# Performance work log

Hardware: AMD Instinct MI355X
Metric: run time of the kernel (lower is better)

Reference implementation:

```python
import jax, jax.numpy as jnp
import numpy as np

NUM_MEMORIES = 4096
HIDDEN_DIM = 64
TEMPERATURE = 0.5
SHRINK_THRES = 0.0025
EPS = 1e-12


def _l2_normalize(v, axis=-1):
    # matches torch F.normalize: v / max(||v||_2, eps)
    n = jnp.sqrt(jnp.sum(v * v, axis=axis, keepdims=True))
    return v / jnp.maximum(n, EPS)


def _hard_shrink_relu(w, lambd):
    # relu(w - lambd) * w / (|w - lambd| + eps)
    d = w - lambd
    return jax.nn.relu(d) * w / (jnp.abs(d) + EPS)


def setup_inputs() -> dict:
    key = jax.random.key(0)
    kx, km = jax.random.split(key)
    x = jax.random.normal(kx, (16, 2048, HIDDEN_DIM), dtype=jnp.float32)
    # xavier_uniform for (num_memories, hidden_dim)
    bound = float(np.sqrt(6.0 / (NUM_MEMORIES + HIDDEN_DIM)))
    memories = jax.random.uniform(km, (NUM_MEMORIES, HIDDEN_DIM), dtype=jnp.float32,
                                  minval=-bound, maxval=bound)
    return {"x": x, "memories": memories}


def reference(x, memories):
    # cosine similarity addressing
    x_n = _l2_normalize(x, axis=-1)                      # [B,S,D]
    m_n = _l2_normalize(memories, axis=-1)               # [M,D]
    logits = jnp.einsum('bsd,md->bsm', x_n, m_n)         # [B,S,M]
    weight = jax.nn.softmax(logits / TEMPERATURE, axis=-1)
    # hard-shrink sparsification + L1 renormalization
    weight = _hard_shrink_relu(weight, SHRINK_THRES)
    l1 = jnp.sum(jnp.abs(weight), axis=-1, keepdims=True)
    weight = weight / jnp.maximum(l1, EPS)
    read = jnp.einsum('bsm,md->bsd', weight, memories)   # [B,S,D]
    return read, weight
```

## Files before the change

### kernel.cpp

```cpp
#include <hip/hip_runtime.h>
#include <hip/hip_bf16.h>


#define NM 4096
#define HD 64
#define NROWS 32768

typedef short bf16x8 __attribute__((ext_vector_type(8)));
typedef float f32x4  __attribute__((ext_vector_type(4)));

__global__ __launch_bounds__(256) void prep_rows(const float* __restrict__ src,
                                                 ushort* __restrict__ dst,
                                                 float scale) {
    const int wave = threadIdx.x >> 6, lane = threadIdx.x & 63;
    const long row = (long)blockIdx.x * 4 + wave;
    float v = src[row * HD + lane];
    float s = v * v;
#pragma unroll
    for (int o = 32; o; o >>= 1) s += __shfl_xor(s, o, 64);
    const float inv = scale / fmaxf(sqrtf(s), 1e-12f);
    __hip_bfloat16 h = __float2bfloat16(v * inv);
    dst[row * HD + lane] = *reinterpret_cast<ushort*>(&h);
}

__global__ __launch_bounds__(256) void prep_m_swz(const float* __restrict__ mem,
                                                  ushort* __restrict__ mbs) {
    const int wave = threadIdx.x >> 6, lane = threadIdx.x & 63;
    const int row = blockIdx.x * 4 + wave;
    float v = mem[row * HD + lane];
    float s = v * v;
#pragma unroll
    for (int o = 32; o; o >>= 1) s += __shfl_xor(s, o, 64);
    const float inv = 1.0f / fmaxf(sqrtf(s), 1e-12f);
    __hip_bfloat16 h = __float2bfloat16(v * inv);
    const int t = row >> 4, c = row & 15;
    const int k = lane;
    const int f = k >> 5, q = (k >> 3) & 3, j = k & 7;
    mbs[(long)t * 1024 + f * 512 + (q * 16 + c) * 8 + j] =
        *reinterpret_cast<ushort*>(&h);
}

__global__ __launch_bounds__(256, 2) void fused_gate(const ushort* __restrict__ xb,
                                                     const ushort* __restrict__ mbs,
                                                     const float* __restrict__ mem,
                                                     float* __restrict__ out_w,
                                                     float* __restrict__ out_read) {
    const int wv = threadIdx.x >> 6, lane = threadIdx.x & 63;
    const int q = lane >> 4, c = lane & 15;
    const int m0 = blockIdx.x * 16;
    const int nbase = wv * 1024;

    __shared__ float sS[4][16];
    __shared__ float sL[4][16];
    __shared__ float sred[4][16][64];
    __shared__ float tile[4][16][68];

    const bf16x8 a0 = *(const bf16x8*)(xb + (long)(m0 + c) * HD + q * 8);
    const bf16x8 a1 = *(const bf16x8*)(xb + (long)(m0 + c) * HD + q * 8 + 32);
    const ushort* mstrip = mbs + (long)(wv * 64) * 1024;

    float tmax[64];
    float sm[4] = {0.0f, 0.0f, 0.0f, 0.0f};
#pragma unroll 4
    for (int i = 0; i < 64; i++) {
        const ushort* mc = mstrip + (long)i * 1024 + lane * 8;
        const bf16x8 b0 = *(const bf16x8*)(mc);
        const bf16x8 b1 = *(const bf16x8*)(mc + 512);
        f32x4 t = {0.0f, 0.0f, 0.0f, 0.0f};
        t = __builtin_amdgcn_mfma_f32_16x16x32_bf16(a0, b0, t, 0, 0, 0);
        t = __builtin_amdgcn_mfma_f32_16x16x32_bf16(a1, b1, t, 0, 0, 0);
        tmax[i] = fmaxf(fmaxf(t[0], t[1]), fmaxf(t[2], t[3]));
#pragma unroll
        for (int r = 0; r < 4; r++) sm[r] += __expf(t[r]);
    }
#pragma unroll
    for (int o = 1; o < 16; o <<= 1)
#pragma unroll
        for (int r = 0; r < 4; r++) sm[r] += __shfl_xor(sm[r], o, 64);
    if (c == 0)
#pragma unroll
        for (int r = 0; r < 4; r++) sS[wv][q * 4 + r] = sm[r];
    __syncthreads();
    float rS[4], tmin = 1e30f;
#pragma unroll
    for (int r = 0; r < 4; r++) {
        const float S = sS[0][q * 4 + r] + sS[1][q * 4 + r] +
                        sS[2][q * 4 + r] + sS[3][q * 4 + r];
        rS[r] = 1.0f / S;
        const float tau = __logf(0.0025f * S) - 1e-3f;
        tmin = fminf(tmin, tau);
    }

    float l1[4] = {0.0f, 0.0f, 0.0f, 0.0f};
    for (int i = 0; i < 64; i++) {
        if (__ballot(tmax[i] > tmin)) {
            const ushort* mc = mstrip + (long)i * 1024 + lane * 8;
            const bf16x8 b0 = *(const bf16x8*)(mc);
            const bf16x8 b1 = *(const bf16x8*)(mc + 512);
            f32x4 t = {0.0f, 0.0f, 0.0f, 0.0f};
            t = __builtin_amdgcn_mfma_f32_16x16x32_bf16(a0, b0, t, 0, 0, 0);
            t = __builtin_amdgcn_mfma_f32_16x16x32_bf16(a1, b1, t, 0, 0, 0);
#pragma unroll
            for (int r = 0; r < 4; r++) {
                float w  = __expf(t[r]) * rS[r];
                float d  = w - 0.0025f;
                l1[r] += __fdividef(fmaxf(d, 0.0f) * w, fabsf(d) + 1e-12f);
            }
        }
    }
#pragma unroll
    for (int o = 1; o < 16; o <<= 1)
#pragma unroll
        for (int r = 0; r < 4; r++) l1[r] += __shfl_xor(l1[r], o, 64);
    if (c == 0)
#pragma unroll
        for (int r = 0; r < 4; r++) sL[wv][q * 4 + r] = l1[r];
    __syncthreads();
    float rL[4];
#pragma unroll
    for (int r = 0; r < 4; r++)
        rL[r] = 1.0f / fmaxf(sL[0][q * 4 + r] + sL[1][q * 4 + r] +
                             sL[2][q * 4 + r] + sL[3][q * 4 + r], 1e-12f);

    float racc[16];
#pragma unroll
    for (int r = 0; r < 16; r++) racc[r] = 0.0f;
    const int row_t = lane >> 4;
    const int c4    = lane & 15;
    const float4 z4 = make_float4(0.0f, 0.0f, 0.0f, 0.0f);

    for (int g = 0; g < 16; g++) {
        unsigned long long dirty = 0;
#pragma unroll
        for (int ii = 0; ii < 4; ii++)
            dirty |= __ballot(tmax[g * 4 + ii] > tmin);
        const int gbase = nbase + g * 64;

        if (!dirty) {
#pragma unroll
            for (int s = 0; s < 4; s++) {
                const int row = s * 4 + row_t;
                *(float4*)(out_w + (long)(m0 + row) * NM + gbase + c4 * 4) = z4;
            }
            continue;
        }

#pragma unroll
        for (int ii = 0; ii < 4; ii++) {
            const int i  = g * 4 + ii;
            const int n0 = nbase + i * 16;
            const ushort* mc = mstrip + (long)i * 1024 + lane * 8;
            const bf16x8 b0 = *(const bf16x8*)(mc);
            const bf16x8 b1 = *(const bf16x8*)(mc + 512);
            f32x4 t = {0.0f, 0.0f, 0.0f, 0.0f};
            t = __builtin_amdgcn_mfma_f32_16x16x32_bf16(a0, b0, t, 0, 0, 0);
            t = __builtin_amdgcn_mfma_f32_16x16x32_bf16(a1, b1, t, 0, 0, 0);
            float wf[4];
#pragma unroll
            for (int r = 0; r < 4; r++) {
                float w  = __expf(t[r]) * rS[r];
                float d  = w - 0.0025f;
                float sh = __fdividef(fmaxf(d, 0.0f) * w, fabsf(d) + 1e-12f);
                wf[r] = sh * rL[r];
                tile[wv][q * 4 + r][ii * 16 + c] = wf[r];
            }

            const bool nz = (wf[0] != 0.0f) | (wf[1] != 0.0f) |
                            (wf[2] != 0.0f) | (wf[3] != 0.0f);
            unsigned long long mask = __ballot(nz);
            while (mask) {
                const int j = __ffsll((long long)mask) - 1;
                mask &= (mask - 1);
                const int qj = j >> 4, cj = j & 15;
                float b0v = __shfl(wf[0], j, 64), b1v = __shfl(wf[1], j, 64);
                float b2v = __shfl(wf[2], j, 64), b3v = __shfl(wf[3], j, 64);
                const float mv = mem[(long)(n0 + cj) * HD + lane];
                switch (qj) {
                    case 0: racc[0]  += b0v * mv; racc[1]  += b1v * mv;
                            racc[2]  += b2v * mv; racc[3]  += b3v * mv; break;
                    case 1: racc[4]  += b0v * mv; racc[5]  += b1v * mv;
                            racc[6]  += b2v * mv; racc[7]  += b3v * mv; break;
                    case 2: racc[8]  += b0v * mv; racc[9]  += b1v * mv;
                            racc[10] += b2v * mv; racc[11] += b3v * mv; break;
                    default: racc[12] += b0v * mv; racc[13] += b1v * mv;
                             racc[14] += b2v * mv; racc[15] += b3v * mv; break;
                }
            }
        }

        __asm__ volatile("s_waitcnt lgkmcnt(0)" ::: "memory");
#pragma unroll
        for (int s = 0; s < 4; s++) {
            const int row = s * 4 + row_t;
            float4 v = *(const float4*)&tile[wv][row][c4 * 4];
            *(float4*)(out_w + (long)(m0 + row) * NM + gbase + c4 * 4) = v;
        }
    }

#pragma unroll
    for (int r = 0; r < 16; r++) sred[wv][r][lane] = racc[r];
    __syncthreads();
#pragma unroll
    for (int rr = 0; rr < 4; rr++) {
        const int row = wv * 4 + rr;
        const float v = sred[0][row][lane] + sred[1][row][lane] +
                        sred[2][row][lane] + sred[3][row][lane];
        out_read[(long)(m0 + row) * HD + lane] = v;
    }
}

extern "C" void kernel_launch(void* const* d_in, const int* in_sizes, int n_in,
                              void* d_out, int out_size, void* d_ws, size_t ws_size,
                              hipStream_t stream) {
    const float* x   = (const float*)d_in[0];
    const float* mem = (const float*)d_in[1];
    ushort* xb       = (ushort*)d_ws;
    ushort* mbs      = xb + (long)NROWS * HD;
    float* out_read  = (float*)d_out;
    float* out_w     = out_read + (long)NROWS * HD;

    prep_rows<<<NROWS / 4, 256, 0, stream>>>(x, xb, 2.0f);
    prep_m_swz<<<NM / 4, 256, 0, stream>>>(mem, mbs);
    fused_gate<<<NROWS / 16, 256, 0, stream>>>(xb, mbs, mem, out_w, out_read);
}
```

Measured before the change: 618.8 us.

## Split fused gate kernel into stats pass and separate weight-write pass

The fused kernel is split into two kernels. k_stats computes the softmax sums, L1 norms and the read output, keeps only one tile max per pair of tiles to save registers, and raises the occupancy hint to 3. It also saves per-row stats and per-wave group masks to workspace. k_write then recomputes the logits for dirty groups and streams the dense weight matrix, with a coalesced fast path for all-zero blocks. The aim is to overlap the large output store with less register pressure, at the cost of an extra launch and recomputing the matmul for dirty groups.

```diff
diff --git a/kernel.cpp b/kernel.cpp
--- a/kernel.cpp
+++ b/kernel.cpp
@@ -40,11 +40,12 @@
         *reinterpret_cast<ushort*>(&h);
 }
 
-__global__ __launch_bounds__(256, 2) void fused_gate(const ushort* __restrict__ xb,
-                                                     const ushort* __restrict__ mbs,
-                                                     const float* __restrict__ mem,
-                                                     float* __restrict__ out_w,
-                                                     float* __restrict__ out_read) {
+__global__ __launch_bounds__(256, 3) void k_stats(const ushort* __restrict__ xb,
+                                                  const ushort* __restrict__ mbs,
+                                                  const float* __restrict__ mem,
+                                                  float2* __restrict__ stats,
+                                                  uint* __restrict__ masks,
+                                                  float* __restrict__ out_read) {
     const int wv = threadIdx.x >> 6, lane = threadIdx.x & 63;
     const int q = lane >> 4, c = lane & 15;
     const int m0 = blockIdx.x * 16;
@@ -53,25 +54,39 @@
     __shared__ float sS[4][16];
     __shared__ float sL[4][16];
     __shared__ float sred[4][16][64];
-    __shared__ float tile[4][16][68];
 
     const bf16x8 a0 = *(const bf16x8*)(xb + (long)(m0 + c) * HD + q * 8);
     const bf16x8 a1 = *(const bf16x8*)(xb + (long)(m0 + c) * HD + q * 8 + 32);
     const ushort* mstrip = mbs + (long)(wv * 64) * 1024;
 
-    float tmax[64];
+    float tmax2[32];
     float sm[4] = {0.0f, 0.0f, 0.0f, 0.0f};
-#pragma unroll 4
-    for (int i = 0; i < 64; i++) {
-        const ushort* mc = mstrip + (long)i * 1024 + lane * 8;
-        const bf16x8 b0 = *(const bf16x8*)(mc);
-        const bf16x8 b1 = *(const bf16x8*)(mc + 512);
-        f32x4 t = {0.0f, 0.0f, 0.0f, 0.0f};
-        t = __builtin_amdgcn_mfma_f32_16x16x32_bf16(a0, b0, t, 0, 0, 0);
-        t = __builtin_amdgcn_mfma_f32_16x16x32_bf16(a1, b1, t, 0, 0, 0);
-        tmax[i] = fmaxf(fmaxf(t[0], t[1]), fmaxf(t[2], t[3]));
-#pragma unroll
-        for (int r = 0; r < 4; r++) sm[r] += __expf(t[r]);
+#pragma unroll 2
+    for (int p = 0; p < 32; p++) {
+        float tm;
+        {
+            const ushort* mc = mstrip + (long)(2 * p) * 1024 + lane * 8;
+            const bf16x8 b0 = *(const bf16x8*)(mc);
+            const bf16x8 b1 = *(const bf16x8*)(mc + 512);
+            f32x4 t = {0.0f, 0.0f, 0.0f, 0.0f};
+            t = __builtin_amdgcn_mfma_f32_16x16x32_bf16(a0, b0, t, 0, 0, 0);
+            t = __builtin_amdgcn_mfma_f32_16x16x32_bf16(a1, b1, t, 0, 0, 0);
+            tm = fmaxf(fmaxf(t[0], t[1]), fmaxf(t[2], t[3]));
+#pragma unroll
+            for (int r = 0; r < 4; r++) sm[r] += __expf(t[r]);
+        }
+        {
+            const ushort* mc = mstrip + (long)(2 * p + 1) * 1024 + lane * 8;
+            const bf16x8 b0 = *(const bf16x8*)(mc);
+            const bf16x8 b1 = *(const bf16x8*)(mc + 512);
+            f32x4 t = {0.0f, 0.0f, 0.0f, 0.0f};
+            t = __builtin_amdgcn_mfma_f32_16x16x32_bf16(a0, b0, t, 0, 0, 0);
+            t = __builtin_amdgcn_mfma_f32_16x16x32_bf16(a1, b1, t, 0, 0, 0);
+            tm = fmaxf(tm, fmaxf(fmaxf(t[0], t[1]), fmaxf(t[2], t[3])));
+#pragma unroll
+            for (int r = 0; r < 4; r++) sm[r] += __expf(t[r]);
+        }
+        tmax2[p] = tm;
     }
 #pragma unroll
     for (int o = 1; o < 16; o <<= 1)
@@ -92,19 +107,22 @@
     }
 
     float l1[4] = {0.0f, 0.0f, 0.0f, 0.0f};
-    for (int i = 0; i < 64; i++) {
-        if (__ballot(tmax[i] > tmin)) {
-            const ushort* mc = mstrip + (long)i * 1024 + lane * 8;
-            const bf16x8 b0 = *(const bf16x8*)(mc);
-            const bf16x8 b1 = *(const bf16x8*)(mc + 512);
-            f32x4 t = {0.0f, 0.0f, 0.0f, 0.0f};
-            t = __builtin_amdgcn_mfma_f32_16x16x32_bf16(a0, b0, t, 0, 0, 0);
-            t = __builtin_amdgcn_mfma_f32_16x16x32_bf16(a1, b1, t, 0, 0, 0);
-#pragma unroll
-            for (int r = 0; r < 4; r++) {
-                float w  = __expf(t[r]) * rS[r];
-                float d  = w - 0.0025f;
-                l1[r] += __fdividef(fmaxf(d, 0.0f) * w, fabsf(d) + 1e-12f);
+    for (int p = 0; p < 32; p++) {
+        if (__ballot(tmax2[p] > tmin)) {
+#pragma unroll
+            for (int h = 0; h < 2; h++) {
+                const ushort* mc = mstrip + (long)(2 * p + h) * 1024 + lane * 8;
+                const bf16x8 b0 = *(const bf16x8*)(mc);
+                const bf16x8 b1 = *(const bf16x8*)(mc + 512);
+                f32x4 t = {0.0f, 0.0f, 0.0f, 0.0f};
+                t = __builtin_amdgcn_mfma_f32_16x16x32_bf16(a0, b0, t, 0, 0, 0);
+                t = __builtin_amdgcn_mfma_f32_16x16x32_bf16(a1, b1, t, 0, 0, 0);
+#pragma unroll
+                for (int r = 0; r < 4; r++) {
+                    float w = __expf(t[r]) * rS[r];
+                    float d = w - 0.0025f;
+                    l1[r] += __fdividef(fmaxf(d, 0.0f) * w, fabsf(d) + 1e-12f);
+                }
             }
         }
     }
@@ -121,30 +139,20 @@
     for (int r = 0; r < 4; r++)
         rL[r] = 1.0f / fmaxf(sL[0][q * 4 + r] + sL[1][q * 4 + r] +
                              sL[2][q * 4 + r] + sL[3][q * 4 + r], 1e-12f);
+    if (wv == 0 && c == 0)
+#pragma unroll
+        for (int r = 0; r < 4; r++)
+            stats[m0 + q * 4 + r] = make_float2(rS[r], rL[r]);
 
     float racc[16];
 #pragma unroll
     for (int r = 0; r < 16; r++) racc[r] = 0.0f;
-    const int row_t = lane >> 4;
-    const int c4    = lane & 15;
-    const float4 z4 = make_float4(0.0f, 0.0f, 0.0f, 0.0f);
-
+    uint gm = 0;
     for (int g = 0; g < 16; g++) {
-        unsigned long long dirty = 0;
-#pragma unroll
-        for (int ii = 0; ii < 4; ii++)
-            dirty |= __ballot(tmax[g * 4 + ii] > tmin);
-        const int gbase = nbase + g * 64;
-
-        if (!dirty) {
-#pragma unroll
-            for (int s = 0; s < 4; s++) {
-                const int row = s * 4 + row_t;
-                *(float4*)(out_w + (long)(m0 + row) * NM + gbase + c4 * 4) = z4;
-            }
-            continue;
-        }
-
+        unsigned long long d0 = __ballot(tmax2[2 * g] > tmin);
+        unsigned long long d1 = __ballot(tmax2[2 * g + 1] > tmin);
+        if (!(d0 | d1)) continue;
+        gm |= 1u << g;
 #pragma unroll
         for (int ii = 0; ii < 4; ii++) {
             const int i  = g * 4 + ii;
@@ -162,9 +170,7 @@
                 float d  = w - 0.0025f;
                 float sh = __fdividef(fmaxf(d, 0.0f) * w, fabsf(d) + 1e-12f);
                 wf[r] = sh * rL[r];
-                tile[wv][q * 4 + r][ii * 16 + c] = wf[r];
-            }
-
+            }
             const bool nz = (wf[0] != 0.0f) | (wf[1] != 0.0f) |
                             (wf[2] != 0.0f) | (wf[3] != 0.0f);
             unsigned long long mask = __ballot(nz);
@@ -187,15 +193,8 @@
                 }
             }
         }
-
-        __asm__ volatile("s_waitcnt lgkmcnt(0)" ::: "memory");
-#pragma unroll
-        for (int s = 0; s < 4; s++) {
-            const int row = s * 4 + row_t;
-            float4 v = *(const float4*)&tile[wv][row][c4 * 4];
-            *(float4*)(out_w + (long)(m0 + row) * NM + gbase + c4 * 4) = v;
-        }
-    }
+    }
+    if (lane == 0) masks[blockIdx.x * 4 + wv] = gm;
 
 #pragma unroll
     for (int r = 0; r < 16; r++) sred[wv][r][lane] = racc[r];
@@ -206,6 +205,81 @@
         const float v = sred[0][row][lane] + sred[1][row][lane] +
                         sred[2][row][lane] + sred[3][row][lane];
         out_read[(long)(m0 + row) * HD + lane] = v;
+    }
+}
+
+__global__ __launch_bounds__(256) void k_write(const ushort* __restrict__ xb,
+                                               const ushort* __restrict__ mbs,
+                                               const float2* __restrict__ stats,
+                                               const uint* __restrict__ masks,
+                                               float* __restrict__ out_w) {
+    const int tid = threadIdx.x;
+    const int wv = tid >> 6, lane = tid & 63;
+    const int q = lane >> 4, c = lane & 15;
+    const int m0 = blockIdx.x * 16;
+
+    __shared__ uint sgm[4];
+    __shared__ float tile[4][16][68];
+
+    if (tid < 4) sgm[tid] = masks[blockIdx.x * 4 + tid];
+    __syncthreads();
+    const uint any = sgm[0] | sgm[1] | sgm[2] | sgm[3];
+    const float4 z4 = make_float4(0.0f, 0.0f, 0.0f, 0.0f);
+
+    if (!any) {
+        float4* base = (float4*)(out_w + (long)m0 * NM);
+#pragma unroll
+        for (int it = 0; it < 64; it++) base[(long)it * 256 + tid] = z4;
+        return;
+    }
+
+    const int nbase = wv * 1024;
+    const uint gm = sgm[wv];
+    const bf16x8 a0 = *(const bf16x8*)(xb + (long)(m0 + c) * HD + q * 8);
+    const bf16x8 a1 = *(const bf16x8*)(xb + (long)(m0 + c) * HD + q * 8 + 32);
+    const ushort* mstrip = mbs + (long)(wv * 64) * 1024;
+    float rS[4], rL[4];
+#pragma unroll
+    for (int r = 0; r < 4; r++) {
+        float2 s = stats[m0 + q * 4 + r];
+        rS[r] = s.x; rL[r] = s.y;
+    }
+    const int row_t = lane >> 4, c4 = lane & 15;
+
+    for (int g = 0; g < 16; g++) {
+        const int gbase = nbase + g * 64;
+        if (!((gm >> g) & 1u)) {
+#pragma unroll
+            for (int s = 0; s < 4; s++) {
+                const int row = s * 4 + row_t;
+                *(float4*)(out_w + (long)(m0 + row) * NM + gbase + c4 * 4) = z4;
+            }
+            continue;
+        }
+#pragma unroll
+        for (int ii = 0; ii < 4; ii++) {
+            const int i = g * 4 + ii;
+            const ushort* mc = mstrip + (long)i * 1024 + lane * 8;
+            const bf16x8 b0 = *(const bf16x8*)(mc);
+            const bf16x8 b1 = *(const bf16x8*)(mc + 512);
+            f32x4 t = {0.0f, 0.0f, 0.0f, 0.0f};
+            t = __builtin_amdgcn_mfma_f32_16x16x32_bf16(a0, b0, t, 0, 0, 0);
+            t = __builtin_amdgcn_mfma_f32_16x16x32_bf16(a1, b1, t, 0, 0, 0);
+#pragma unroll
+            for (int r = 0; r < 4; r++) {
+                float w  = __expf(t[r]) * rS[r];
+                float d  = w - 0.0025f;
+                float sh = __fdividef(fmaxf(d, 0.0f) * w, fabsf(d) + 1e-12f);
+                tile[wv][q * 4 + r][ii * 16 + c] = sh * rL[r];
+            }
+        }
+        __asm__ volatile("s_waitcnt lgkmcnt(0)" ::: "memory");
+#pragma unroll
+        for (int s = 0; s < 4; s++) {
+            const int row = s * 4 + row_t;
+            float4 v = *(const float4*)&tile[wv][row][c4 * 4];
+            *(float4*)(out_w + (long)(m0 + row) * NM + gbase + c4 * 4) = v;
+        }
     }
 }
 
@@ -216,10 +290,13 @@
     const float* mem = (const float*)d_in[1];
     ushort* xb       = (ushort*)d_ws;
     ushort* mbs      = xb + (long)NROWS * HD;
+    float2* stats    = (float2*)(mbs + (long)NM * HD);
+    uint*   masks    = (uint*)(stats + NROWS);
     float* out_read  = (float*)d_out;
     float* out_w     = out_read + (long)NROWS * HD;
 
     prep_rows<<<NROWS / 4, 256, 0, stream>>>(x, xb, 2.0f);
     prep_m_swz<<<NM / 4, 256, 0, stream>>>(mem, mbs);
-    fused_gate<<<NROWS / 16, 256, 0, stream>>>(xb, mbs, mem, out_w, out_read);
-}
+    k_stats<<<NROWS / 16, 256, 0, stream>>>(xb, mbs, mem, stats, masks, out_read);
+    k_write<<<NROWS / 16, 256, 0, stream>>>(xb, mbs, stats, masks, out_w);
+}
```

New measurement: 601.5 us. 2.8% less time.
